# Kernel optimization log

Measured on AMD Instinct MI355X. Metric: run time of the kernel, lower is better.

## Reference

```python
import jax, jax.numpy as jnp
import numpy as np

B, D, T, H, L_PRED = 256, 64, 336, 512, 96


def _cell(x, h, c, W_ih, W_hh, b_ih, b_hh):
    # PyTorch LSTM gate order: i, f, g, o
    g = x @ W_ih.T + h @ W_hh.T + (b_ih + b_hh)
    i, f, gg, o = jnp.split(g, 4, axis=-1)
    c2 = jax.nn.sigmoid(f) * c + jax.nn.sigmoid(i) * jnp.tanh(gg)
    h2 = jax.nn.sigmoid(o) * jnp.tanh(c2)
    return h2, c2


def setup_inputs() -> dict:
    key = jax.random.key(0)
    ks = jax.random.split(key, 11)
    s = 0.05
    f32 = jnp.float32
    return {
        "x": jax.random.normal(ks[0], (B, D, T), f32),
        "W_ih0": jax.random.normal(ks[1], (4 * H, D), f32) * s,
        "W_hh0": jax.random.normal(ks[2], (4 * H, H), f32) * s,
        "b_ih0": jax.random.normal(ks[3], (4 * H,), f32) * s,
        "b_hh0": jax.random.normal(ks[4], (4 * H,), f32) * s,
        "W_ih1": jax.random.normal(ks[5], (4 * H, H), f32) * s,
        "W_hh1": jax.random.normal(ks[6], (4 * H, H), f32) * s,
        "b_ih1": jax.random.normal(ks[7], (4 * H,), f32) * s,
        "b_hh1": jax.random.normal(ks[8], (4 * H,), f32) * s,
        "W_out": jax.random.normal(ks[9], (D, H), f32) * s,
        "b_out": jax.random.normal(ks[10], (D,), f32) * s,
    }


def reference(x, W_ih0, W_hh0, b_ih0, b_hh0, W_ih1, W_hh1, b_ih1, b_hh1, W_out, b_out):
    xt = jnp.transpose(x, (0, 2, 1))  # (B, T, D) after the module's permute
    b = xt.shape[0]
    h0 = jnp.zeros((b, H), xt.dtype)
    c0 = jnp.zeros((b, H), xt.dtype)
    h1 = jnp.zeros((b, H), xt.dtype)
    c1 = jnp.zeros((b, H), xt.dtype)

    def enc_step(carry, x_t):
        h0, c0, h1, c1 = carry
        h0, c0 = _cell(x_t, h0, c0, W_ih0, W_hh0, b_ih0, b_hh0)
        h1, c1 = _cell(h0, h1, c1, W_ih1, W_hh1, b_ih1, b_hh1)
        return (h0, c0, h1, c1), None

    (h0, c0, h1, c1), _ = jax.lax.scan(enc_step, (h0, c0, h1, c1),
                                       jnp.transpose(xt, (1, 0, 2)))  # (T, B, D)
    global_feat = h1  # lstm_out[:, -1, :] == final top-layer hidden state

    dec_in = jnp.zeros((b, D), xt.dtype)

    def dec_step(carry, _):
        h0, c0, h1, c1, inp = carry
        h0, c0 = _cell(inp, h0, c0, W_ih0, W_hh0, b_ih0, b_hh0)
        h1, c1 = _cell(h0, h1, c1, W_ih1, W_hh1, b_ih1, b_hh1)
        pred = h1 @ W_out.T + b_out  # (B, D)
        return (h0, c0, h1, c1, pred), pred

    _, preds = jax.lax.scan(dec_step, (h0, c0, h1, c1, dec_in), None, length=L_PRED)
    preds = jnp.transpose(preds, (1, 2, 0))  # (B, D, pred_len) == permute(0,2,1)
    return global_feat, preds
```

## Files before the change

kernel.cpp:

```cpp
#include <hip/hip_runtime.h>

typedef unsigned short u16;
typedef __attribute__((ext_vector_type(8))) short short8;
typedef __attribute__((ext_vector_type(4))) float f32x4;

#define AXR __ATOMIC_RELAXED, __HIP_MEMORY_SCOPE_AGENT

__device__ __forceinline__ float bf2f(u16 v){
  union { unsigned u; float f; } t; t.u = ((unsigned)v) << 16; return t.f;
}
__device__ __forceinline__ u16 f2bf(float f){
  union { float f; unsigned u; } t; t.f = f;
  unsigned u = t.u;
  return (u16)((u + 0x7fffu + ((u >> 16) & 1u)) >> 16);
}
struct HiLo { short hi, lo; };
__device__ __forceinline__ HiLo split1(float v){
  HiLo r;
  u16 h = f2bf(v);
  r.hi = (short)h;
  r.lo = (short)f2bf(v - bf2f(h));
  return r;
}
__device__ __forceinline__ void ldw8s(const float* __restrict__ p, short8& hi, short8& lo){
  #pragma unroll
  for (int j = 0; j < 8; ++j){ HiLo s = split1(p[j]); hi[j] = s.hi; lo[j] = s.lo; }
}

#define MFMA(acc, a, b) acc = __builtin_amdgcn_mfma_f32_16x16x32_bf16(a, b, acc, 0,0,0)
#define SMACC(acc, ah, al, bh, bl) do{ MFMA(acc, ah, bh); MFMA(acc, ah, bl); MFMA(acc, al, bh); }while(0)

__global__ void wcvt(const float* __restrict__ s, u16* __restrict__ hi, int n){
  int i = blockIdx.x * blockDim.x + threadIdx.x;
  if (i < n) hi[i] = f2bf(s[i]);
}

__global__ void __launch_bounds__(256) wcomb_k(
    const float* __restrict__ Wih0, const float* __restrict__ Wout,
    const float* __restrict__ bout, const float* __restrict__ bih0,
    const float* __restrict__ bhh0,
    u16* __restrict__ Wch, float* __restrict__ bb)
{
  __shared__ float wl[8*64];
  __shared__ float bo[64];
  const int wg = blockIdx.x, tid = threadIdx.x;
  const int r0 = wg*8;
  for (int i = tid; i < 512; i += 256) wl[i] = Wih0[(r0 + (i >> 6))*64 + (i & 63)];
  if (tid < 64) bo[tid] = bout[tid];
  __syncthreads();
  if (tid < 8){
    int n = r0 + tid;
    float a = bih0[n] + bhh0[n];
    #pragma unroll 8
    for (int d = 0; d < 64; ++d) a += wl[tid*64 + d]*bo[d];
    bb[n] = a;
  }
  #pragma unroll
  for (int jj = 0; jj < 2; ++jj){
    int j = tid + jj*256;
    float acc[8] = {0,0,0,0,0,0,0,0};
    for (int d = 0; d < 64; ++d){
      float wv = Wout[d*512 + j];
      #pragma unroll
      for (int r = 0; r < 8; ++r) acc[r] += wl[r*64 + d]*wv;
    }
    #pragma unroll
    for (int r = 0; r < 8; ++r) Wch[(r0 + r)*512 + j] = f2bf(acc[r]);
  }
}

__device__ __forceinline__ void gbar(unsigned* bar, unsigned phase){
  __syncthreads();
  if (threadIdx.x == 0){
    __threadfence();
    const unsigned gg = (unsigned)blockIdx.x >> 4;
    unsigned old = __hip_atomic_fetch_add(bar + 64 + gg*32, 1u, AXR);
    if (old == phase*16u - 1u){
      unsigned r = __hip_atomic_fetch_add(bar, 1u, AXR);
      if (r == phase*16u - 1u)
        __hip_atomic_store(bar + 32, phase, AXR);
    }
    while (__hip_atomic_load(bar + 32, AXR) < phase)
      __builtin_amdgcn_s_sleep(2);
    __threadfence();
  }
  __syncthreads();
}

__device__ __forceinline__ void xbar(unsigned* bar, unsigned phase,
                                     unsigned xcd, unsigned pop, unsigned nx){
  __syncthreads();
  if (threadIdx.x == 0){
    unsigned old = __hip_atomic_fetch_add(bar + 832 + xcd*32, 1u, AXR);
    const bool leader = (old == phase*pop - 1u);
    if (leader){
      asm volatile("buffer_wbl2 sc1\n\ts_waitcnt vmcnt(0)" ::: "memory");
      unsigned r = __hip_atomic_fetch_add(bar + 1344, 1u, AXR);
      if (r == phase*nx - 1u)
        __hip_atomic_store(bar + 1376, phase, AXR);
    }
    while (__hip_atomic_load(bar + 1376, AXR) < phase)
      __builtin_amdgcn_s_sleep(2);
    if (leader){
      asm volatile("buffer_inv sc1\n\ts_waitcnt vmcnt(0)" ::: "memory");
      __hip_atomic_store(bar + 1088 + xcd*32, phase, AXR);
    } else {
      while (__hip_atomic_load(bar + 1088 + xcd*32, AXR) < phase)
        __builtin_amdgcn_s_sleep(1);
      asm volatile("buffer_inv\n\ts_waitcnt vmcnt(0)" ::: "memory");
    }
  }
  __syncthreads();
}

__device__ __forceinline__ void fbar(unsigned* bar, int g, int cg,
                                     unsigned phase, int tid){
  __syncthreads();
  unsigned* flags = bar + 4096 + g*1024;
  if (tid == 0)
    __hip_atomic_store(flags + cg*32, phase, AXR);
  if (tid < 64){
    const int i = tid & 31;
    while (__hip_atomic_load(flags + i*32, AXR) < phase)
      __builtin_amdgcn_s_sleep(1);
    asm volatile("buffer_inv\n\ts_waitcnt vmcnt(0)" ::: "memory");
  }
  __syncthreads();
}

__device__ __forceinline__ short8 lds8(const u16* base, int r, int kelem, int rowbytes){
  int bo = r*rowbytes + ((kelem*2) ^ ((r & 7) << 4));
  return *(const short8*)((const char*)base + bo);
}

__device__ __forceinline__ void stage_ld(const u16* __restrict__ gh,
                                         short8* r, int tid){
  #pragma unroll
  for (int i = 0; i < 8; ++i)
    r[i] = *(const short8*)(gh + (tid + i*256)*8);
}
__device__ __forceinline__ void stage_wr(const short8* r, u16* sh, int tid){
  #pragma unroll
  for (int i = 0; i < 8; ++i){
    int e = (tid + i*256)*8;
    int row = e >> 9, col = e & 511;
    int bo = row*1024 + ((col*2) ^ ((row & 7) << 4));
    *(short8*)((char*)sh + bo) = r[i];
  }
}

__global__ void __launch_bounds__(256, 1) lstm_persist(
    const float* __restrict__ x,
    const float* __restrict__ Whh0, const float* __restrict__ Wih0,
    const u16* __restrict__ W1ih_h, const u16* __restrict__ W1hh_h,
    const u16* __restrict__ Wcmb_h, const float* __restrict__ bb,
    const float* __restrict__ bih0, const float* __restrict__ bhh0,
    const float* __restrict__ bih1, const float* __restrict__ bhh1,
    const float* __restrict__ Wout, const float* __restrict__ bout,
    float* __restrict__ out, unsigned* __restrict__ cnt,
    u16* __restrict__ h0h0, u16* __restrict__ h0h1,
    u16* __restrict__ h1h0, u16* __restrict__ h1h1)
{
  __shared__ u16 hstA[16384], hstB[16384];
  __shared__ float glA[32*68];
  __shared__ float glB[32*68];
  __shared__ float pr[256];
  __shared__ float bs0[64], bs1[64], bsd[64];
  __shared__ unsigned s_rank, s_pop, s_nx, s_all;

  u16* xst_h = (u16*)glA;
  u16* xst_l = (u16*)glA + 2048;

  const int wg = blockIdx.x, tid = threadIdx.x;
  const int lane = tid & 63, wv = tid >> 6;
  const int cI = lane & 15;
  const int kc = (lane >> 4) << 3;
  const int rl = wv*16 + cI;

  unsigned xcd;
  asm volatile("s_getreg_b32 %0, hwreg(HW_REG_XCC_ID)" : "=s"(xcd));
  xcd &= 7u;
  if (tid == 0)
    s_rank = __hip_atomic_fetch_add(cnt + 576 + xcd*32, 1u, AXR);
  gbar(cnt, 1);
  if (tid == 0){
    unsigned nxl = 0, allc = 1;
    for (int i = 0; i < 8; ++i){
      unsigned pv = __hip_atomic_load(cnt + 576 + i*32, AXR);
      nxl += (pv != 0u) ? 1u : 0u;
      if (pv != 32u) allc = 0u;
    }
    s_pop = __hip_atomic_load(cnt + 576 + xcd*32, AXR);
    s_nx  = nxl;
    s_all = allc;
  }
  __syncthreads();
  const unsigned pop = s_pop, nx = s_nx;
  const bool allco = (s_all != 0u);
  const int g  = allco ? (int)xcd    : (wg & 7);
  const int cg = allco ? (int)s_rank : (wg >> 3);
  const int b0 = g*32;

  if (tid < 64){
    int n = ((tid >> 4) << 9) + cg*16 + (tid & 15);
    bs0[tid] = bih0[n] + bhh0[n];
    bs1[tid] = bih1[n] + bhh1[n];
    bsd[tid] = bb[n];
  }
  const int nrow = wv*512 + cg*16 + cI;
  const int nb = nrow*512 + kc;
  short8 w1ih_r[16], w1hh_r[16], wcmb_r[16], w0hh_r[16];
  #pragma unroll
  for (int ks = 0; ks < 16; ++ks){
    w1ih_r[ks] = *(const short8*)(W1ih_h + nb + ks*32);
    w1hh_r[ks] = *(const short8*)(W1hh_h + nb + ks*32);
    wcmb_r[ks] = *(const short8*)(Wcmb_h + nb + ks*32);
    short8 t;
    #pragma unroll
    for (int j = 0; j < 8; ++j) t[j] = (short)f2bf(Whh0[nb + ks*32 + j]);
    w0hh_r[ks] = t;
  }
  short8 w0ih_rh[2], w0ih_rl[2];
  #pragma unroll
  for (int ks = 0; ks < 2; ++ks){
    short8 th, tl;
    #pragma unroll
    for (int j = 0; j < 8; ++j){
      HiLo s = split1(Wih0[nrow*64 + ks*32 + kc + j]);
      th[j] = s.hi; tl[j] = s.lo;
    }
    w0ih_rh[ks] = th; w0ih_rl[ks] = tl;
  }
  __syncthreads();

  u16* H0h[2] = { h0h0, h0h1 };
  u16* H1h[2] = { h1h0, h1h1 };

  float c0r[2] = {0.f, 0.f}, c1r[2] = {0.f, 0.f};
  unsigned ep = 0;
  const int rb_ = (lane >> 4) << 2;
  const int hoff = b0*512;

  #define LDA(buf, kk, a0h_, a1h_) \
    short8 a0h_ = lds8(buf, cI, kc + (kk), 1024); \
    short8 a1h_ = lds8(buf, cI + 16, kc + (kk), 1024);

  #define CELL(GL, CREG, HDST, GF) { \
    u16* Hh_ = (HDST); \
    _Pragma("unroll") \
    for (int q = 0; q < 2; ++q){ \
      int e = tid + q*256; \
      int m = e >> 4, col = e & 15; \
      float iv = GL[m*68 + col]; \
      float fv = GL[m*68 + 16 + col]; \
      float gv = GL[m*68 + 32 + col]; \
      float ov = GL[m*68 + 48 + col]; \
      float si = 1.f/(1.f + expf(-iv)); \
      float sf = 1.f/(1.f + expf(-fv)); \
      float so = 1.f/(1.f + expf(-ov)); \
      float cn = sf*CREG[q] + si*tanhf(gv); \
      CREG[q] = cn; \
      float h = so*tanhf(cn); \
      int gi = (b0 + m)*512 + cg*16 + col; \
      Hh_[gi] = f2bf(h); \
      if (GF) ((float*)(GF))[gi] = h; \
    } }

  for (int k = 0; k <= 336; ++k){
    const int p0 = k & 1;

    short8 r0s[8], r1s[8];
    float xr[8];
    stage_ld(H0h[p0^1] + hoff, r0s, tid);
    if (k >= 1) stage_ld(H1h[p0] + hoff, r1s, tid);
    if (k < 336){
      #pragma unroll
      for (int i = 0; i < 8; ++i){
        int e = tid + i*256;
        xr[i] = x[(b0 + (e >> 6))*21504 + (e & 63)*336 + k];
      }
    }
    stage_wr(r0s, hstA, tid);
    if (k >= 1) stage_wr(r1s, hstB, tid);
    if (k < 336){
      #pragma unroll
      for (int i = 0; i < 8; ++i){
        int e = tid + i*256;
        int bb_ = e >> 6, d = e & 63;
        HiLo s = split1(xr[i]);
        int bo = bb_*128 + ((d*2) ^ ((bb_ & 7) << 4));
        *(u16*)((char*)xst_h + bo) = (u16)s.hi;
        *(u16*)((char*)xst_l + bo) = (u16)s.lo;
      }
    }
    __syncthreads();

    f32x4 A0 = {0,0,0,0}, A1 = {0,0,0,0};
    f32x4 B0 = {0,0,0,0}, B1 = {0,0,0,0};
    if (k < 336){
      #pragma unroll
      for (int ks = 0; ks < 2; ++ks){
        int kk = ks*32 + kc;
        short8 a0h = lds8(xst_h, cI, kk, 128);
        short8 a0l = lds8(xst_l, cI, kk, 128);
        short8 a1h = lds8(xst_h, cI + 16, kk, 128);
        short8 a1l = lds8(xst_l, cI + 16, kk, 128);
        SMACC(A0, a0h, a0l, w0ih_rh[ks], w0ih_rl[ks]);
        SMACC(A1, a1h, a1l, w0ih_rh[ks], w0ih_rl[ks]);
      }
    }
    #pragma unroll
    for (int ks = 0; ks < 16; ++ks){
      int kk = ks*32;
      LDA(hstA, kk, a0h, a1h)
      MFMA(A0, a0h, w0hh_r[ks]);
      MFMA(A1, a1h, w0hh_r[ks]);
      MFMA(B0, a0h, w1ih_r[ks]);
      MFMA(B1, a1h, w1ih_r[ks]);
    }
    if (k >= 1){
      #pragma unroll
      for (int ks = 0; ks < 16; ++ks){
        int kk = ks*32;
        LDA(hstB, kk, a0h, a1h)
        MFMA(B0, a0h, w1hh_r[ks]);
        MFMA(B1, a1h, w1hh_r[ks]);
      }
    }

    __syncthreads();
    #pragma unroll
    for (int r = 0; r < 4; ++r){
      glA[(rb_ + r)*68 + rl]      = A0[r] + bs0[rl];
      glA[(16 + rb_ + r)*68 + rl] = A1[r] + bs0[rl];
    }
    if (k >= 1){
      #pragma unroll
      for (int r = 0; r < 4; ++r){
        glB[(rb_ + r)*68 + rl]      = B0[r] + bs1[rl];
        glB[(16 + rb_ + r)*68 + rl] = B1[r] + bs1[rl];
      }
    }
    __syncthreads();
    CELL(glA, c0r, H0h[p0], (float*)nullptr)
    if (k >= 1)  CELL(glB, c1r, H1h[p0^1], (k == 336) ? out : nullptr)
    ++ep;
    if (allco) fbar(cnt, g, cg, ep, tid); else xbar(cnt, ep, xcd, pop, nx);
  }

  {
    short8 r0s[8], r1s[8];
    stage_ld(H0h[0] + hoff, r0s, tid);
    stage_ld(H1h[1] + hoff, r1s, tid);
    stage_wr(r0s, hstA, tid);
    stage_wr(r1s, hstB, tid);
    __syncthreads();
    f32x4 B0 = {0,0,0,0}, B1 = {0,0,0,0};
    #pragma unroll
    for (int ks = 0; ks < 16; ++ks){
      int kk = ks*32;
      LDA(hstA, kk, a0h, a1h)
      MFMA(B0, a0h, w1ih_r[ks]);
      MFMA(B1, a1h, w1ih_r[ks]);
    }
    #pragma unroll
    for (int ks = 0; ks < 16; ++ks){
      int kk = ks*32;
      LDA(hstB, kk, a0h, a1h)
      MFMA(B0, a0h, w1hh_r[ks]);
      MFMA(B1, a1h, w1hh_r[ks]);
    }
    __syncthreads();
    #pragma unroll
    for (int r = 0; r < 4; ++r){
      glB[(rb_ + r)*68 + rl]      = B0[r] + bs1[rl];
      glB[(16 + rb_ + r)*68 + rl] = B1[r] + bs1[rl];
    }
    __syncthreads();
    CELL(glB, c1r, H1h[0], (float*)nullptr)
    ++ep;
    if (allco) fbar(cnt, g, cg, ep, tid); else xbar(cnt, ep, xcd, pop, nx);
  }

  for (int t = 337; t < 432; ++t){
    const int p = t & 1;

    {
      short8 r0s[8], r1s[8];
      stage_ld(H1h[p^1] + hoff, r0s, tid);
      stage_ld(H0h[p^1] + hoff, r1s, tid);
      stage_wr(r0s, hstA, tid);
      stage_wr(r1s, hstB, tid);
      __syncthreads();
      f32x4 A0 = {0,0,0,0}, A1 = {0,0,0,0};
      #pragma unroll
      for (int ks = 0; ks < 16; ++ks){
        int kk = ks*32;
        LDA(hstA, kk, a0h, a1h)
        MFMA(A0, a0h, wcmb_r[ks]);
        MFMA(A1, a1h, wcmb_r[ks]);
      }
      #pragma unroll
      for (int ks = 0; ks < 16; ++ks){
        int kk = ks*32;
        LDA(hstB, kk, a0h, a1h)
        MFMA(A0, a0h, w0hh_r[ks]);
        MFMA(A1, a1h, w0hh_r[ks]);
      }
      {
        const int d = tid & 63, kq = tid >> 6;
        float part = 0.f;
        const float* wr = Wout + d*512 + kq*128;
        #pragma unroll 4
        for (int kk = 0; kk < 128; kk += 8){
          short8 hv = lds8(hstA, cg, kq*128 + kk, 1024);
          #pragma unroll
          for (int j = 0; j < 8; ++j)
            part += bf2f((u16)hv[j]) * wr[kk + j];
        }
        pr[d*4 + kq] = part;
        __syncthreads();
        if (tid < 64){
          float v = pr[tid*4] + pr[tid*4+1] + pr[tid*4+2] + pr[tid*4+3] + bout[tid];
          out[131072 + ((b0 + cg)*64 + tid)*96 + (t - 337)] = v;
        }
      }
      __syncthreads();
      #pragma unroll
      for (int r = 0; r < 4; ++r){
        glA[(rb_ + r)*68 + rl]      = A0[r] + bsd[rl];
        glA[(16 + rb_ + r)*68 + rl] = A1[r] + bsd[rl];
      }
      __syncthreads();
      CELL(glA, c0r, H0h[p], (float*)nullptr)
      ++ep;
      if (allco) fbar(cnt, g, cg, ep, tid); else xbar(cnt, ep, xcd, pop, nx);
    }

    {
      short8 r0s[8], r1s[8];
      stage_ld(H0h[p] + hoff, r0s, tid);
      stage_ld(H1h[p^1] + hoff, r1s, tid);
      stage_wr(r0s, hstA, tid);
      stage_wr(r1s, hstB, tid);
      __syncthreads();
      f32x4 B0 = {0,0,0,0}, B1 = {0,0,0,0};
      #pragma unroll
      for (int ks = 0; ks < 16; ++ks){
        int kk = ks*32;
        LDA(hstA, kk, a0h, a1h)
        MFMA(B0, a0h, w1ih_r[ks]);
        MFMA(B1, a1h, w1ih_r[ks]);
      }
      #pragma unroll
      for (int ks = 0; ks < 16; ++ks){
        int kk = ks*32;
        LDA(hstB, kk, a0h, a1h)
        MFMA(B0, a0h, w1hh_r[ks]);
        MFMA(B1, a1h, w1hh_r[ks]);
      }
      __syncthreads();
      #pragma unroll
      for (int r = 0; r < 4; ++r){
        glB[(rb_ + r)*68 + rl]      = B0[r] + bs1[rl];
        glB[(16 + rb_ + r)*68 + rl] = B1[r] + bs1[rl];
      }
      __syncthreads();
      CELL(glB, c1r, H1h[p], (float*)nullptr)
      ++ep;
      if (allco) fbar(cnt, g, cg, ep, tid); else xbar(cnt, ep, xcd, pop, nx);
    }
  }
  #undef LDA
  #undef CELL
}

__global__ void __launch_bounds__(256) pred_last(
    const u16* __restrict__ h1hi,
    const float* __restrict__ Wout, const float* __restrict__ bout,
    float* __restrict__ out)
{
  const int wg = blockIdx.x, tid = threadIdx.x;
  const int bsub = tid >> 6, d = tid & 63;
  const int b = wg*4 + bsub;
  float acc = bout[d];
  const u16* hH = h1hi + b*512;
  const float* wr = Wout + d*512;
  #pragma unroll 8
  for (int k = 0; k < 512; k += 8){
    short8 hv = *(const short8*)(hH + k);
    #pragma unroll
    for (int j = 0; j < 8; ++j)
      acc += bf2f((u16)hv[j]) * wr[k + j];
  }
  out[131072 + (b*64 + d)*96 + 95] = acc;
}

__device__ __forceinline__ void cell_epilogue_fb(
    float* gl, const float* bs, float* __restrict__ cbuf,
    u16* __restrict__ hhi, u16* __restrict__ hlo,
    float* __restrict__ gfout, int mrow, int jblk,
    const f32x4& a0, const f32x4& a1, int wv, int lane, int tid)
{
  __syncthreads();
  const int rbase = wv*16 + ((lane >> 4) << 2);
  const int cI = lane & 15;
  #pragma unroll
  for (int r = 0; r < 4; ++r){
    gl[(rbase+r)*33 + cI]      = a0[r] + bs[cI];
    gl[(rbase+r)*33 + 16 + cI] = a1[r] + bs[16 + cI];
  }
  __syncthreads();
  #pragma unroll
  for (int q = 0; q < 2; ++q){
    int e = tid + q*256;
    int m = e >> 3, jj = e & 7;
    float iv = gl[m*33 + jj];
    float fv = gl[m*33 + 8 + jj];
    float gv = gl[m*33 + 16 + jj];
    float ov = gl[m*33 + 24 + jj];
    float si = 1.f/(1.f + expf(-iv));
    float sf = 1.f/(1.f + expf(-fv));
    float so = 1.f/(1.f + expf(-ov));
    int gi = (mrow*64 + m)*512 + jblk*8 + jj;
    float cn = sf*cbuf[gi] + si*tanhf(gv);
    cbuf[gi] = cn;
    float h = so*tanhf(cn);
    u16 hh = f2bf(h);
    hhi[gi] = hh;
    hlo[gi] = f2bf(h - bf2f(hh));
    if (gfout) gfout[gi] = h;
  }
}

template<bool ENC>
__global__ void __launch_bounds__(256) l0_fb(
    const float* __restrict__ x,
    const u16* __restrict__ predhi, const u16* __restrict__ predlo,
    const float* __restrict__ Wihf, const float* __restrict__ Whhf,
    const float* __restrict__ bih, const float* __restrict__ bhh,
    const u16* __restrict__ hphi, const u16* __restrict__ hplo,
    u16* __restrict__ hnhi, u16* __restrict__ hnlo,
    float* __restrict__ c0, int t)
{
  __shared__ float gl[64*33];
  __shared__ float bs[32];
  const int wg = blockIdx.x, tid = threadIdx.x;
  const int mrow = wg & 3, jblk = wg >> 2;
  const int lane = tid & 63, wv = tid >> 6;
  if (tid < 32){
    int n = ((tid >> 3) << 9) + jblk*8 + (tid & 7);
    bs[tid] = bih[n] + bhh[n];
  }
  const int ar = mrow*64 + wv*16 + (lane & 15);
  const int kc = (lane >> 4) << 3;
  const int cI = lane & 15;
  const int n0 = ((cI >> 3) << 9) + jblk*8 + (cI & 7);
  const int n1 = n0 + 1024;

  f32x4 acc0 = {0,0,0,0}, acc1 = {0,0,0,0};
  #pragma unroll
  for (int ks = 0; ks < 2; ++ks){
    int k = ks*32 + kc;
    short8 ah, al;
    if (ENC){
      const float* xb = x + ar*21504 + t;
      #pragma unroll
      for (int j = 0; j < 8; ++j){ HiLo s = split1(xb[(k + j)*336]); ah[j] = s.hi; al[j] = s.lo; }
    } else {
      ah = *(const short8*)(predhi + ar*64 + k);
      al = *(const short8*)(predlo + ar*64 + k);
    }
    short8 bh0, bl0, bh1, bl1;
    ldw8s(Wihf + n0*64 + k, bh0, bl0);
    ldw8s(Wihf + n1*64 + k, bh1, bl1);
    SMACC(acc0, ah, al, bh0, bl0);
    SMACC(acc1, ah, al, bh1, bl1);
  }
  const u16* hH = hphi + ar*512 + kc;
  const u16* hL = hplo + ar*512 + kc;
  #pragma unroll 4
  for (int ks = 0; ks < 16; ++ks){
    int k = ks*32;
    short8 ah = *(const short8*)(hH + k);
    short8 al = *(const short8*)(hL + k);
    short8 bh0, bl0, bh1, bl1;
    ldw8s(Whhf + n0*512 + kc + k, bh0, bl0);
    ldw8s(Whhf + n1*512 + kc + k, bh1, bl1);
    SMACC(acc0, ah, al, bh0, bl0);
    SMACC(acc1, ah, al, bh1, bl1);
  }
  cell_epilogue_fb(gl, bs, c0, hnhi, hnlo, nullptr, mrow, jblk, acc0, acc1, wv, lane, tid);
}

__global__ void __launch_bounds__(256) l1_fb(
    const float* __restrict__ Wihf, const float* __restrict__ Whhf,
    const float* __restrict__ bih, const float* __restrict__ bhh,
    const u16* __restrict__ h0hi, const u16* __restrict__ h0lo,
    const u16* __restrict__ h1phi, const u16* __restrict__ h1plo,
    u16* __restrict__ h1nhi, u16* __restrict__ h1nlo,
    float* __restrict__ c1, float* __restrict__ gfout)
{
  __shared__ float gl[64*33];
  __shared__ float bs[32];
  const int wg = blockIdx.x, tid = threadIdx.x;
  const int mrow = wg & 3, jblk = wg >> 2;
  const int lane = tid & 63, wv = tid >> 6;
  if (tid < 32){
    int n = ((tid >> 3) << 9) + jblk*8 + (tid & 7);
    bs[tid] = bih[n] + bhh[n];
  }
  const int ar = mrow*64 + wv*16 + (lane & 15);
  const int kc = (lane >> 4) << 3;
  const int cI = lane & 15;
  const int n0 = ((cI >> 3) << 9) + jblk*8 + (cI & 7);
  const int n1 = n0 + 1024;

  f32x4 acc0 = {0,0,0,0}, acc1 = {0,0,0,0};
  {
    const u16* hH = h0hi + ar*512 + kc;
    const u16* hL = h0lo + ar*512 + kc;
    #pragma unroll 4
    for (int ks = 0; ks < 16; ++ks){
      int k = ks*32;
      short8 ah = *(const short8*)(hH + k);
      short8 al = *(const short8*)(hL + k);
      short8 bh0, bl0, bh1, bl1;
      ldw8s(Wihf + n0*512 + kc + k, bh0, bl0);
      ldw8s(Wihf + n1*512 + kc + k, bh1, bl1);
      SMACC(acc0, ah, al, bh0, bl0);
      SMACC(acc1, ah, al, bh1, bl1);
    }
  }
  {
    const u16* hH = h1phi + ar*512 + kc;
    const u16* hL = h1plo + ar*512 + kc;
    #pragma unroll 4
    for (int ks = 0; ks < 16; ++ks){
      int k = ks*32;
      short8 ah = *(const short8*)(hH + k);
      short8 al = *(const short8*)(hL + k);
      short8 bh0, bl0, bh1, bl1;
      ldw8s(Whhf + n0*512 + kc + k, bh0, bl0);
      ldw8s(Whhf + n1*512 + kc + k, bh1, bl1);
      SMACC(acc0, ah, al, bh0, bl0);
      SMACC(acc1, ah, al, bh1, bl1);
    }
  }
  cell_epilogue_fb(gl, bs, c1, h1nhi, h1nlo, gfout, mrow, jblk, acc0, acc1, wv, lane, tid);
}

__global__ void __launch_bounds__(256) pred_fb(
    const u16* __restrict__ h1hi, const u16* __restrict__ h1lo,
    const float* __restrict__ Wout, const float* __restrict__ bout,
    u16* __restrict__ predhi, u16* __restrict__ predlo,
    float* __restrict__ out, int l)
{
  const int wg = blockIdx.x, tid = threadIdx.x;
  const int bsub = tid >> 6, d = tid & 63;
  const int b = wg*4 + bsub;
  float acc = bout[d];
  const u16* hH = h1hi + b*512;
  const u16* hL = h1lo + b*512;
  const float* wr = Wout + d*512;
  #pragma unroll 8
  for (int k = 0; k < 512; k += 8){
    short8 hv = *(const short8*)(hH + k);
    short8 lv = *(const short8*)(hL + k);
    #pragma unroll
    for (int j = 0; j < 8; ++j)
      acc += (bf2f((u16)hv[j]) + bf2f((u16)lv[j])) * wr[k + j];
  }
  HiLo s = split1(acc);
  predhi[b*64 + d] = (u16)s.hi;
  predlo[b*64 + d] = (u16)s.lo;
  out[131072 + (b*64 + d)*96 + l] = acc;
}

extern "C" void kernel_launch(void* const* d_in, const int* in_sizes, int n_in,
                              void* d_out, int out_size, void* d_ws, size_t ws_size,
                              hipStream_t stream)
{
  const float* x    = (const float*)d_in[0];
  const float* Wih0 = (const float*)d_in[1];
  const float* Whh0 = (const float*)d_in[2];
  const float* bih0 = (const float*)d_in[3];
  const float* bhh0 = (const float*)d_in[4];
  const float* Wih1 = (const float*)d_in[5];
  const float* Whh1 = (const float*)d_in[6];
  const float* bih1 = (const float*)d_in[7];
  const float* bhh1 = (const float*)d_in[8];
  const float* Wout = (const float*)d_in[9];
  const float* bout = (const float*)d_in[10];
  float* out = (float*)d_out;

  char* ws = (char*)d_ws;
  u16* h0h[2] = { (u16*)(ws + 0),       (u16*)(ws + 262144) };
  u16* h0l[2] = { (u16*)(ws + 524288),  (u16*)(ws + 786432) };
  u16* h1h[2] = { (u16*)(ws + 1048576), (u16*)(ws + 1310720) };
  u16* h1l[2] = { (u16*)(ws + 1572864), (u16*)(ws + 1835008) };
  unsigned* cnt = (unsigned*)(ws + 2097152);
  u16* Wcmb_h = (u16*)(ws + 2162688);
  u16* W1ih_h = Wcmb_h + 1048576;
  u16* W1hh_h = W1ih_h + 1048576;
  float* bb   = (float*)(W1hh_h + 1048576);
  const size_t NEED = 2162688u + 3u*2097152u + 8192u;
  float* fb_c0 = (float*)(ws + 2162688);
  float* fb_c1 = (float*)(ws + 2686976);
  u16* predh   = (u16*)(ws + 3211264);
  u16* predl   = (u16*)(ws + 3244032);
  const bool ps = (ws_size >= NEED);

  (void)hipMemsetAsync(d_ws, 0, 3276800, stream);

  if (ps){
    wcomb_k<<<dim3(256), dim3(256), 0, stream>>>(Wih0, Wout, bout, bih0, bhh0,
                                                 Wcmb_h, bb);
    wcvt<<<dim3(4096), dim3(256), 0, stream>>>(Wih1, W1ih_h, 1048576);
    wcvt<<<dim3(4096), dim3(256), 0, stream>>>(Whh1, W1hh_h, 1048576);
    lstm_persist<<<dim3(256), dim3(256), 0, stream>>>(
        x, Whh0, Wih0, W1ih_h, W1hh_h, Wcmb_h, bb,
        bih0, bhh0, bih1, bhh1, Wout, bout, out, cnt,
        h0h[0], h0h[1], h1h[0], h1h[1]);
    pred_last<<<dim3(64), dim3(256), 0, stream>>>(h1h[1], Wout, bout, out);
  } else {
    for (int t = 0; t < 432; ++t){
      const int p = t & 1;
      float* gf = (t == 335) ? out : (float*)nullptr;
      if (t < 336)
        l0_fb<true><<<dim3(256), dim3(256), 0, stream>>>(
            x, predh, predl, Wih0, Whh0, bih0, bhh0,
            h0h[p^1], h0l[p^1], h0h[p], h0l[p], fb_c0, t);
      else
        l0_fb<false><<<dim3(256), dim3(256), 0, stream>>>(
            x, predh, predl, Wih0, Whh0, bih0, bhh0,
            h0h[p^1], h0l[p^1], h0h[p], h0l[p], fb_c0, t);
      l1_fb<<<dim3(256), dim3(256), 0, stream>>>(
          Wih1, Whh1, bih1, bhh1, h0h[p], h0l[p],
          h1h[p^1], h1l[p^1], h1h[p], h1l[p], fb_c1, gf);
      if (t >= 336)
        pred_fb<<<dim3(64), dim3(256), 0, stream>>>(
            h1h[p], h1l[p], Wout, bout, predh, predl, out, t - 336);
    }
  }
}
```

Baseline: 3.758 ms.

## Prefetch next-step x into dedicated LDS, drop syncs, use fast gate math

Moves the x staging into its own LDS buffers so it no longer aliases glA, and prefetches the next timestep's x slice during the current step, writing it after the cell update. This takes the global x load off the step's critical path and lets the __syncthreads before each gate-scratch write be removed. Sigmoid and tanh now use __expf and hardware reciprocal instead of expf, tanhf and a division. The fast math is less precise, and the removed barriers rely on the glA/glB buffers no longer being shared with other data.

```diff
diff --git a/kernel.cpp b/kernel.cpp
--- a/kernel.cpp
+++ b/kernel.cpp
@@ -25,6 +25,13 @@
 __device__ __forceinline__ void ldw8s(const float* __restrict__ p, short8& hi, short8& lo){
   #pragma unroll
   for (int j = 0; j < 8; ++j){ HiLo s = split1(p[j]); hi[j] = s.hi; lo[j] = s.lo; }
+}
+
+__device__ __forceinline__ float fsig(float v){
+  return __builtin_amdgcn_rcpf(1.f + __expf(-v));
+}
+__device__ __forceinline__ float ftanh(float v){
+  return 1.f - 2.f*__builtin_amdgcn_rcpf(__expf(2.f*v) + 1.f);
 }
 
 #define MFMA(acc, a, b) acc = __builtin_amdgcn_mfma_f32_16x16x32_bf16(a, b, acc, 0,0,0)
@@ -162,14 +169,12 @@
     u16* __restrict__ h1h0, u16* __restrict__ h1h1)
 {
   __shared__ u16 hstA[16384], hstB[16384];
+  __shared__ u16 xsh[2048], xsl[2048];
   __shared__ float glA[32*68];
   __shared__ float glB[32*68];
   __shared__ float pr[256];
   __shared__ float bs0[64], bs1[64], bsd[64];
   __shared__ unsigned s_rank, s_pop, s_nx, s_all;
-
-  u16* xst_h = (u16*)glA;
-  u16* xst_l = (u16*)glA + 2048;
 
   const int wg = blockIdx.x, tid = threadIdx.x;
   const int lane = tid & 63, wv = tid >> 6;
@@ -231,6 +236,16 @@
     }
     w0ih_rh[ks] = th; w0ih_rl[ks] = tl;
   }
+
+  #pragma unroll
+  for (int i = 0; i < 8; ++i){
+    int e = tid + i*256;
+    int bb_ = e >> 6, d = e & 63;
+    HiLo s = split1(x[(b0 + bb_)*21504 + d*336 + 0]);
+    int bo = bb_*128 + ((d*2) ^ ((bb_ & 7) << 4));
+    *(u16*)((char*)xsh + bo) = (u16)s.hi;
+    *(u16*)((char*)xsl + bo) = (u16)s.lo;
+  }
   __syncthreads();
 
   u16* H0h[2] = { h0h0, h0h1 };
@@ -255,12 +270,9 @@
       float fv = GL[m*68 + 16 + col]; \
       float gv = GL[m*68 + 32 + col]; \
       float ov = GL[m*68 + 48 + col]; \
-      float si = 1.f/(1.f + expf(-iv)); \
-      float sf = 1.f/(1.f + expf(-fv)); \
-      float so = 1.f/(1.f + expf(-ov)); \
-      float cn = sf*CREG[q] + si*tanhf(gv); \
+      float cn = fsig(fv)*CREG[q] + fsig(iv)*ftanh(gv); \
       CREG[q] = cn; \
-      float h = so*tanhf(cn); \
+      float h = fsig(ov)*ftanh(cn); \
       int gi = (b0 + m)*512 + cg*16 + col; \
       Hh_[gi] = f2bf(h); \
       if (GF) ((float*)(GF))[gi] = h; \
@@ -270,29 +282,10 @@
     const int p0 = k & 1;
 
     short8 r0s[8], r1s[8];
-    float xr[8];
     stage_ld(H0h[p0^1] + hoff, r0s, tid);
     if (k >= 1) stage_ld(H1h[p0] + hoff, r1s, tid);
-    if (k < 336){
-      #pragma unroll
-      for (int i = 0; i < 8; ++i){
-        int e = tid + i*256;
-        xr[i] = x[(b0 + (e >> 6))*21504 + (e & 63)*336 + k];
-      }
-    }
     stage_wr(r0s, hstA, tid);
     if (k >= 1) stage_wr(r1s, hstB, tid);
-    if (k < 336){
-      #pragma unroll
-      for (int i = 0; i < 8; ++i){
-        int e = tid + i*256;
-        int bb_ = e >> 6, d = e & 63;
-        HiLo s = split1(xr[i]);
-        int bo = bb_*128 + ((d*2) ^ ((bb_ & 7) << 4));
-        *(u16*)((char*)xst_h + bo) = (u16)s.hi;
-        *(u16*)((char*)xst_l + bo) = (u16)s.lo;
-      }
-    }
     __syncthreads();
 
     f32x4 A0 = {0,0,0,0}, A1 = {0,0,0,0};
@@ -301,10 +294,10 @@
       #pragma unroll
       for (int ks = 0; ks < 2; ++ks){
         int kk = ks*32 + kc;
-        short8 a0h = lds8(xst_h, cI, kk, 128);
-        short8 a0l = lds8(xst_l, cI, kk, 128);
-        short8 a1h = lds8(xst_h, cI + 16, kk, 128);
-        short8 a1l = lds8(xst_l, cI + 16, kk, 128);
+        short8 a0h = lds8(xsh, cI, kk, 128);
+        short8 a0l = lds8(xsl, cI, kk, 128);
+        short8 a1h = lds8(xsh, cI + 16, kk, 128);
+        short8 a1l = lds8(xsl, cI + 16, kk, 128);
         SMACC(A0, a0h, a0l, w0ih_rh[ks], w0ih_rl[ks]);
         SMACC(A1, a1h, a1l, w0ih_rh[ks], w0ih_rl[ks]);
       }
@@ -328,7 +321,16 @@
       }
     }
 
-    __syncthreads();
+    float xr[8];
+    const bool ldx = (k + 1 < 336);
+    if (ldx){
+      #pragma unroll
+      for (int i = 0; i < 8; ++i){
+        int e = tid + i*256;
+        xr[i] = x[(b0 + (e >> 6))*21504 + (e & 63)*336 + (k + 1)];
+      }
+    }
+
     #pragma unroll
     for (int r = 0; r < 4; ++r){
       glA[(rb_ + r)*68 + rl]      = A0[r] + bs0[rl];
@@ -344,6 +346,17 @@
     __syncthreads();
     CELL(glA, c0r, H0h[p0], (float*)nullptr)
     if (k >= 1)  CELL(glB, c1r, H1h[p0^1], (k == 336) ? out : nullptr)
+    if (ldx){
+      #pragma unroll
+      for (int i = 0; i < 8; ++i){
+        int e = tid + i*256;
+        int bb_ = e >> 6, d = e & 63;
+        HiLo s = split1(xr[i]);
+        int bo = bb_*128 + ((d*2) ^ ((bb_ & 7) << 4));
+        *(u16*)((char*)xsh + bo) = (u16)s.hi;
+        *(u16*)((char*)xsl + bo) = (u16)s.lo;
+      }
+    }
     ++ep;
     if (allco) fbar(cnt, g, cg, ep, tid); else xbar(cnt, ep, xcd, pop, nx);
   }
@@ -370,7 +383,6 @@
       MFMA(B0, a0h, w1hh_r[ks]);
       MFMA(B1, a1h, w1hh_r[ks]);
     }
-    __syncthreads();
     #pragma unroll
     for (int r = 0; r < 4; ++r){
       glB[(rb_ + r)*68 + rl]      = B0[r] + bs1[rl];
@@ -425,7 +437,6 @@
           out[131072 + ((b0 + cg)*64 + tid)*96 + (t - 337)] = v;
         }
       }
-      __syncthreads();
       #pragma unroll
       for (int r = 0; r < 4; ++r){
         glA[(rb_ + r)*68 + rl]      = A0[r] + bsd[rl];
@@ -459,7 +470,6 @@
         MFMA(B0, a0h, w1hh_r[ks]);
         MFMA(B1, a1h, w1hh_r[ks]);
       }
-      __syncthreads();
       #pragma unroll
       for (int r = 0; r < 4; ++r){
         glB[(rb_ + r)*68 + rl]      = B0[r] + bs1[rl];
```

Measured after the change: 3.169 ms. 1.19x faster.
